# Optimization experiments

Hardware: AMD Instinct MI355X
Metric: run time of the kernel (lower is better)

## Reference

```python
import jax, jax.numpy as jnp
import numpy as np

DIM = 3072
HEADS = 24
HEAD_DIM = 128
SEQ = 4096
BATCH = 1
EPS = 1e-6


def setup_inputs() -> dict:
    key = jax.random.key(0)
    ks = jax.random.split(key, 12)
    s = 1.0 / np.sqrt(DIM)
    return {
        "hidden_states": jax.random.normal(ks[0], (BATCH, SEQ, DIM), dtype=jnp.float32),
        "cos": jax.random.uniform(ks[1], (SEQ, HEAD_DIM), dtype=jnp.float32, minval=-1.0, maxval=1.0),
        "sin": jax.random.uniform(ks[2], (SEQ, HEAD_DIM), dtype=jnp.float32, minval=-1.0, maxval=1.0),
        "Wq": jax.random.normal(ks[3], (DIM, HEADS * HEAD_DIM), dtype=jnp.float32) * s,
        "bq": jax.random.normal(ks[4], (HEADS * HEAD_DIM,), dtype=jnp.float32) * 0.02,
        "Wk": jax.random.normal(ks[5], (DIM, HEADS * HEAD_DIM), dtype=jnp.float32) * s,
        "bk": jax.random.normal(ks[6], (HEADS * HEAD_DIM,), dtype=jnp.float32) * 0.02,
        "Wv": jax.random.normal(ks[7], (DIM, HEADS * HEAD_DIM), dtype=jnp.float32) * s,
        "bv": jax.random.normal(ks[8], (HEADS * HEAD_DIM,), dtype=jnp.float32) * 0.02,
        "gq": jnp.ones((HEAD_DIM,), dtype=jnp.float32),
        "gk": jnp.ones((HEAD_DIM,), dtype=jnp.float32),
    }


def _rms_norm(x, g):
    # RMSNorm over last dim (head_dim), learnable scale g
    var = jnp.mean(jnp.square(x), axis=-1, keepdims=True)
    return x * jax.lax.rsqrt(var + EPS) * g


def _apply_rope(x, cos, sin):
    # x: [B, S, H, D]; cos/sin: [S, D]. Interleaved-pair rotation (Flux style).
    xr = x.reshape(*x.shape[:-1], HEAD_DIM // 2, 2)
    x_rot = jnp.stack((-xr[..., 1], xr[..., 0]), axis=-1).reshape(x.shape)
    c = cos[None, :, None, :]
    s = sin[None, :, None, :]
    return x * c + x_rot * s


def reference(hidden_states, cos, sin, Wq, bq, Wk, bk, Wv, bv, gq, gk):
    B, S, _ = hidden_states.shape
    q = (hidden_states @ Wq + bq).reshape(B, S, HEADS, HEAD_DIM)
    k = (hidden_states @ Wk + bk).reshape(B, S, HEADS, HEAD_DIM)
    v = (hidden_states @ Wv + bv).reshape(B, S, HEADS, HEAD_DIM)
    q = _apply_rope(_rms_norm(q, gq), cos, sin)
    k = _apply_rope(_rms_norm(k, gk), cos, sin)
    scale = 1.0 / jnp.sqrt(jnp.asarray(HEAD_DIM, dtype=q.dtype))
    scores = jnp.einsum("bqhd,bkhd->bhqk", q, k) * scale  # [B, H, S, S]
    probs = jax.nn.softmax(scores, axis=-1)
    out = jnp.einsum("bhqk,bkhd->bqhd", probs, v)  # [B, S, H, D]
    return out.reshape(B, S, HEADS * HEAD_DIM)
```

## Files before the change

kernel.cpp:

```cpp
#include <hip/hip_runtime.h>
#include <hip/hip_bf16.h>
#include <stdint.h>

#define DIM 3072
#define SEQ 4096
#define NH 24
#define HD 128

typedef __hip_bfloat16 bf16;
typedef __bf16 bfv8 __attribute__((ext_vector_type(8)));
typedef float f32x4 __attribute__((ext_vector_type(4)));
typedef float f32x16 __attribute__((ext_vector_type(16)));
typedef unsigned short us4 __attribute__((ext_vector_type(4)));
typedef unsigned short us8 __attribute__((ext_vector_type(8)));

template <int N> struct ic { static constexpr int value = N; };

__device__ __forceinline__ void async16(void* lds, const void* g) {
  __builtin_amdgcn_global_load_lds((const __attribute__((address_space(1))) void*)g,
                                   (__attribute__((address_space(3))) void*)lds, 16, 0, 0);
}

__device__ __forceinline__ unsigned short f2bf(float f) {
  unsigned int u = __builtin_bit_cast(unsigned int, f);
  u += 0x7fffu + ((u >> 16) & 1u);
  return (unsigned short)(u >> 16);
}
__device__ __forceinline__ float bf2f(unsigned short b) {
  return __builtin_bit_cast(float, (unsigned int)b << 16);
}
__device__ __forceinline__ unsigned int cvtpk(float lo, float hi) {
  unsigned int r;
  asm("v_cvt_pk_bf16_f32 %0, %1, %2" : "=v"(r) : "v"(lo), "v"(hi));
  return r;
}
__device__ __forceinline__ void pl32swap(unsigned int& a, unsigned int& b) {
  asm volatile("v_permlane32_swap_b32 %0, %1" : "+v"(a), "+v"(b));
}
#if __has_builtin(__builtin_amdgcn_exp2f)
__device__ __forceinline__ float fexp2(float x) { return __builtin_amdgcn_exp2f(x); }
#else
__device__ __forceinline__ float fexp2(float x) { return exp2f(x); }
#endif

#define MFMA16(a, b, c) __builtin_amdgcn_mfma_f32_16x16x32_bf16((a), (b), (c), 0, 0, 0)
#define MFMA32(a, b, c) __builtin_amdgcn_mfma_f32_32x32x16_bf16((a), (b), (c), 0, 0, 0)

__global__ __launch_bounds__(256) void k_cast(const float4* __restrict__ in,
                                              us4* __restrict__ o, int n4) {
  int i = blockIdx.x * 256 + threadIdx.x;
  if (i >= n4) return;
  float4 v = in[i];
  us4 r;
  r.x = f2bf(v.x); r.y = f2bf(v.y); r.z = f2bf(v.z); r.w = f2bf(v.w);
  o[i] = r;
}

__global__ __launch_bounds__(256) void k_transW(const float* __restrict__ W0,
    const float* __restrict__ W1, const float* __restrict__ W2,
    unsigned short* __restrict__ T0, unsigned short* __restrict__ T1,
    unsigned short* __restrict__ T2) {
  int z = blockIdx.z;
  const float* W = (z == 0) ? W0 : (z == 1) ? W1 : W2;
  unsigned short* T = (z == 0) ? T0 : (z == 1) ? T1 : T2;
  int kb = blockIdx.y * 64;
  int nb = blockIdx.x * 64;
  __shared__ float tile[64 * 64];
  int t = threadIdx.x;
#pragma unroll
  for (int p = 0; p < 4; ++p) {
    int cid = p * 256 + t;
    int row = cid >> 4, c4 = cid & 15;
    int slot = (c4 + (row >> 3)) & 15;
    float4 v = *(const float4*)&W[(size_t)(kb + row) * DIM + nb + c4 * 4];
    *(float4*)&tile[row * 64 + slot * 4] = v;
  }
  __syncthreads();
#pragma unroll
  for (int p = 0; p < 2; ++p) {
    int cid = p * 256 + t;
    int nl = cid >> 3, c8 = cid & 7;
    us8 o;
#pragma unroll
    for (int j = 0; j < 8; ++j) {
      int k = c8 * 8 + j;
      int slot = ((nl >> 2) + (k >> 3)) & 15;
      o[j] = f2bf(tile[k * 64 + slot * 4 + (nl & 3)]);
    }
    *(us8*)&T[(size_t)(nb + nl) * DIM + kb + c8 * 8] = o;
  }
}

__global__ __launch_bounds__(256, 3) void k_gemm(const unsigned short* __restrict__ A,
    const unsigned short* __restrict__ B0, const unsigned short* __restrict__ B1,
    const unsigned short* __restrict__ B2, const float* __restrict__ c0,
    const float* __restrict__ c1, const float* __restrict__ c2,
    const float* __restrict__ cosT, const float* __restrict__ sinT,
    const float* __restrict__ gq, const float* __restrict__ gk,
    unsigned short* __restrict__ o0, unsigned short* __restrict__ o1,
    unsigned short* __restrict__ o2) {
  const int b = blockIdx.x;
  const int yb = b % 32;
  const int r2b = b / 32;
  const int xb = r2b % 24;
  const int z = r2b / 24;
  const unsigned short* Bt = (z == 0) ? B0 : (z == 1) ? B1 : B2;
  const float* bias = (z == 0) ? c0 : (z == 1) ? c1 : c2;
  unsigned short* outp = (z == 0) ? o0 : (z == 1) ? o1 : o2;
  const int nb = xb * 128;
  const int mb = yb * 128;
  const int t = threadIdx.x;
  const int w = t >> 6, l = t & 63;
  const int wr = w >> 1, wc = w & 1;
  const int lq = l & 15, lg = l >> 4;
  __shared__ unsigned short lA[128 * 64];
  __shared__ unsigned short lB[128 * 64];
  __shared__ float lds_sq[128 * 2];
  f32x4 acc[4][4];
#pragma unroll
  for (int i = 0; i < 4; ++i)
#pragma unroll
    for (int j = 0; j < 4; ++j) acc[i][j] = (f32x4){0.f, 0.f, 0.f, 0.f};

  for (int kb = 0; kb < DIM; kb += 64) {
    __syncthreads();
#pragma unroll
    for (int r = 0; r < 4; ++r) {
      int row = (w * 4 + r) * 8 + (l >> 3);
      int sl = (l & 7) ^ (row & 7);
      async16(&lA[(w * 4 + r) * 512], A + (size_t)(mb + row) * DIM + kb + sl * 8);
      async16(&lB[(w * 4 + r) * 512], Bt + (size_t)(nb + row) * DIM + kb + sl * 8);
    }
    __syncthreads();
#pragma unroll
    for (int kc = 0; kc < 2; ++kc) {
      bfv8 af[4], bfv[4];
#pragma unroll
      for (int mf = 0; mf < 4; ++mf) {
        int row = wr * 64 + mf * 16 + lq;
        af[mf] = *(const bfv8*)&lA[row * 64 + (((kc * 4 + lg) ^ (row & 7)) * 8)];
      }
#pragma unroll
      for (int nf = 0; nf < 4; ++nf) {
        int row = wc * 64 + nf * 16 + lq;
        bfv[nf] = *(const bfv8*)&lB[row * 64 + (((kc * 4 + lg) ^ (row & 7)) * 8)];
      }
#pragma unroll
      for (int mf = 0; mf < 4; ++mf)
#pragma unroll
        for (int nf = 0; nf < 4; ++nf)
          acc[mf][nf] = MFMA16(af[mf], bfv[nf], acc[mf][nf]);
    }
  }

  float bv4[4];
#pragma unroll
  for (int nf = 0; nf < 4; ++nf) bv4[nf] = bias[nb + wc * 64 + nf * 16 + lq];
#pragma unroll
  for (int mf = 0; mf < 4; ++mf)
#pragma unroll
    for (int nf = 0; nf < 4; ++nf)
#pragma unroll
      for (int r = 0; r < 4; ++r) acc[mf][nf][r] += bv4[nf];

  const int hh = nb >> 7;
  unsigned short* obase0 = outp + (size_t)hh * SEQ * HD;

  if (z == 2) {
#pragma unroll
    for (int nf = 0; nf < 4; ++nf) {
      int dd = wc * 64 + nf * 16 + lq;
#pragma unroll
      for (int mf = 0; mf < 4; ++mf) {
        int srow = mb + wr * 64 + mf * 16 + lg * 4;
#pragma unroll
        for (int r = 0; r < 4; ++r)
          obase0[(size_t)(srow + r) * HD + dd] = f2bf(acc[mf][nf][r]);
      }
    }
    return;
  }

  float psum[4][4];
#pragma unroll
  for (int mf = 0; mf < 4; ++mf)
#pragma unroll
    for (int r = 0; r < 4; ++r) {
      float p = acc[mf][0][r] * acc[mf][0][r];
      p += acc[mf][1][r] * acc[mf][1][r];
      p += acc[mf][2][r] * acc[mf][2][r];
      p += acc[mf][3][r] * acc[mf][3][r];
      p += __shfl_xor(p, 1);
      p += __shfl_xor(p, 2);
      p += __shfl_xor(p, 4);
      p += __shfl_xor(p, 8);
      psum[mf][r] = p;
    }
  if (lq == 0) {
#pragma unroll
    for (int mf = 0; mf < 4; ++mf)
#pragma unroll
      for (int r = 0; r < 4; ++r)
        lds_sq[(wr * 64 + mf * 16 + lg * 4 + r) * 2 + wc] = psum[mf][r];
  }
  __syncthreads();

  const float* g = (z == 0) ? gq : gk;
  float gvec[4];
#pragma unroll
  for (int nf = 0; nf < 4; ++nf) gvec[nf] = g[wc * 64 + nf * 16 + lq];
  const float qs = (z == 0) ? 0.1275174373f : 1.0f;

#pragma unroll
  for (int mf = 0; mf < 4; ++mf)
#pragma unroll
    for (int r = 0; r < 4; ++r) {
      int row = wr * 64 + mf * 16 + lg * 4 + r;
      float tot = lds_sq[row * 2] + lds_sq[row * 2 + 1];
      float rrv = rsqrtf(tot * (1.0f / 128.0f) + 1e-6f);
      int s = mb + row;
#pragma unroll
      for (int nf = 0; nf < 4; ++nf) {
        int dd = wc * 64 + nf * 16 + lq;
        float y = acc[mf][nf][r] * rrv * gvec[nf];
        float yp = __shfl_xor(y, 1);
        float cc = cosT[s * HD + dd], sn = sinT[s * HD + dd];
        float o = (lq & 1) ? fmaf(yp, sn, y * cc) : fmaf(-yp, sn, y * cc);
        obase0[(size_t)s * HD + dd] = f2bf(o * qs);
      }
    }
}

__global__ __launch_bounds__(256) void k_transV(const unsigned short* __restrict__ vb,
                                                unsigned short* __restrict__ vt) {
  int hh = blockIdx.y;
  int sb = blockIdx.x * 64;
  __shared__ unsigned short tile[64 * 128];
  int t = threadIdx.x;
#pragma unroll
  for (int p = 0; p < 4; ++p) {
    int cid = p * 256 + t;
    int row = cid >> 4, c = cid & 15;
    int slot = (c + (row >> 3)) & 15;
    us8 v = *(const us8*)&vb[((size_t)hh * SEQ + sb + row) * HD + c * 8];
    *(us8*)&tile[row * 128 + slot * 8] = v;
  }
  __syncthreads();
#pragma unroll
  for (int p = 0; p < 4; ++p) {
    int cid = p * 256 + t;
    int d = cid >> 3, c8 = cid & 7;
    us8 o;
#pragma unroll
    for (int j = 0; j < 8; ++j) {
      int s = c8 * 8 + j;
      int slot = ((d >> 3) + (s >> 3)) & 15;
      o[j] = tile[s * 128 + slot * 8 + (d & 7)];
    }
    *(us8*)&vt[((size_t)hh * HD + d) * SEQ + sb + c8 * 8] = o;
  }
}

__global__ __launch_bounds__(256, 2) void k_attn(const unsigned short* __restrict__ qg,
    const unsigned short* __restrict__ kg, const unsigned short* __restrict__ vtg,
    float* __restrict__ outp) {
  const int bflat = blockIdx.x;
  const int h = bflat % 24;
  const int qb0 = (bflat / 24) * 128;
  const int t = threadIdx.x;
  const int w = t >> 6, l = t & 63;
  const int l31 = l & 31, hi = l >> 5;

  __shared__ unsigned short lKf[2 * 8192];
  __shared__ unsigned short lVf[2 * 8192];

  bfv8 qf[8];
  {
    const unsigned short* qrow = qg + ((size_t)h * SEQ + qb0 + w * 32 + l31) * HD + hi * 8;
#pragma unroll
    for (int ks = 0; ks < 8; ++ks) qf[ks] = *(const bfv8*)(qrow + ks * 16);
  }

  int kidx[8], vidx[4][2];
#pragma unroll
  for (int ks = 0; ks < 8; ++ks)
    kidx[ks] = l31 * 128 + (((ks * 2 + hi) ^ (l31 & 7) ^ ((l31 >> 3) & 1)) * 8);
#pragma unroll
  for (int dt = 0; dt < 4; ++dt)
#pragma unroll
    for (int ksub = 0; ksub < 2; ++ksub)
      vidx[dt][ksub] =
          (dt * 32 + l31) * 32 + (((ksub * 2 + hi) ^ (l31 & 3) ^ ((l31 >> 2) & 3)) * 8);

  const unsigned short *kp0, *kp1, *vp0, *vp1;
  {
    int kr0 = w * 4 + (l >> 4), kr1 = 16 + kr0;
    kp0 = kg + ((size_t)h * SEQ + kr0) * HD + (((l & 15) ^ (kr0 & 7) ^ ((kr0 >> 3) & 1)) * 8);
    kp1 = kg + ((size_t)h * SEQ + kr1) * HD + (((l & 15) ^ (kr1 & 7) ^ ((kr1 >> 3) & 1)) * 8);
    int vr0 = w * 16 + (l >> 2), vr1 = 64 + vr0;
    vp0 = vtg + ((size_t)h * HD + vr0) * SEQ + (((l & 3) ^ (vr0 & 3) ^ ((vr0 >> 2) & 3)) * 8);
    vp1 = vtg + ((size_t)h * HD + vr1) * SEQ + (((l & 3) ^ (vr1 & 3) ^ ((vr1 >> 2) & 3)) * 8);
  }

#define STAGE(B)                                                              \
  do {                                                                        \
    async16(&lKf[(B) * 8192 + w * 512], kp0);                                 \
    async16(&lKf[(B) * 8192 + 2048 + w * 512], kp1);                          \
    async16(&lKf[(B) * 8192 + 4096 + w * 512], kp0 + 32 * HD);                \
    async16(&lKf[(B) * 8192 + 6144 + w * 512], kp1 + 32 * HD);                \
    async16(&lVf[(B) * 8192 + w * 512], vp0);                                 \
    async16(&lVf[(B) * 8192 + 2048 + w * 512], vp1);                          \
    async16(&lVf[(B) * 8192 + 4096 + w * 512], vp0 + 32);                     \
    async16(&lVf[(B) * 8192 + 6144 + w * 512], vp1 + 32);                     \
    kp0 += 64 * HD; kp1 += 64 * HD; vp0 += 64; vp1 += 64;                     \
  } while (0)

  f32x16 oacc[4];
#pragma unroll
  for (int dt = 0; dt < 4; ++dt)
#pragma unroll
    for (int r = 0; r < 16; ++r) oacc[dt][r] = 0.f;
  float l_run = 0.f;

  STAGE(0);

  auto phase = [&](auto bufc, auto stagec) {
    constexpr int CUR = decltype(bufc)::value;
    constexpr int DOSTAGE = decltype(stagec)::value;
    asm volatile("s_waitcnt vmcnt(0)" ::: "memory");
    __builtin_amdgcn_s_barrier();
    __builtin_amdgcn_sched_barrier(0);
    if constexpr (DOSTAGE) STAGE(CUR ^ 1);
    __builtin_amdgcn_sched_barrier(0);

    f32x16 sa, sb;
#pragma unroll
    for (int r = 0; r < 16; ++r) { sa[r] = 0.f; sb[r] = 0.f; }
    __builtin_amdgcn_s_setprio(1);
#pragma unroll
    for (int ks = 0; ks < 8; ++ks) {
      bfv8 kfa = *(const bfv8*)&lKf[CUR * 8192 + kidx[ks]];
      bfv8 kfb = *(const bfv8*)&lKf[CUR * 8192 + 4096 + kidx[ks]];
      sa = MFMA32(kfa, qf[ks], sa);
      sb = MFMA32(kfb, qf[ks], sb);
    }
    __builtin_amdgcn_s_setprio(0);

#pragma unroll
    for (int r = 0; r < 16; ++r) { sa[r] = fexp2(sa[r]); sb[r] = fexp2(sb[r]); }
    {
      float a0 = (sa[0] + sa[1]) + (sa[2] + sa[3]);
      float a1 = (sa[4] + sa[5]) + (sa[6] + sa[7]);
      float a2 = (sa[8] + sa[9]) + (sa[10] + sa[11]);
      float a3 = (sa[12] + sa[13]) + (sa[14] + sa[15]);
      float b0 = (sb[0] + sb[1]) + (sb[2] + sb[3]);
      float b1 = (sb[4] + sb[5]) + (sb[6] + sb[7]);
      float b2 = (sb[8] + sb[9]) + (sb[10] + sb[11]);
      float b3 = (sb[12] + sb[13]) + (sb[14] + sb[15]);
      l_run += ((a0 + a1) + (a2 + a3)) + ((b0 + b1) + (b2 + b3));
    }

    bfv8 paA[2], paB[2];
    {
      unsigned int a0 = cvtpk(sa[0], sa[1]), a1 = cvtpk(sa[2], sa[3]);
      unsigned int b0 = cvtpk(sa[4], sa[5]), b1 = cvtpk(sa[6], sa[7]);
      unsigned int c0 = cvtpk(sa[8], sa[9]), c1 = cvtpk(sa[10], sa[11]);
      unsigned int d0 = cvtpk(sa[12], sa[13]), d1 = cvtpk(sa[14], sa[15]);
      pl32swap(a0, b0); pl32swap(a1, b1); pl32swap(c0, d0); pl32swap(c1, d1);
      paA[0] = __builtin_bit_cast(bfv8, make_uint4(a0, a1, b0, b1));
      paA[1] = __builtin_bit_cast(bfv8, make_uint4(c0, c1, d0, d1));
      a0 = cvtpk(sb[0], sb[1]); a1 = cvtpk(sb[2], sb[3]);
      b0 = cvtpk(sb[4], sb[5]); b1 = cvtpk(sb[6], sb[7]);
      c0 = cvtpk(sb[8], sb[9]); c1 = cvtpk(sb[10], sb[11]);
      d0 = cvtpk(sb[12], sb[13]); d1 = cvtpk(sb[14], sb[15]);
      pl32swap(a0, b0); pl32swap(a1, b1); pl32swap(c0, d0); pl32swap(c1, d1);
      paB[0] = __builtin_bit_cast(bfv8, make_uint4(a0, a1, b0, b1));
      paB[1] = __builtin_bit_cast(bfv8, make_uint4(c0, c1, d0, d1));
    }

    __builtin_amdgcn_s_setprio(1);
#pragma unroll
    for (int dt = 0; dt < 4; ++dt) {
#pragma unroll
      for (int ksub = 0; ksub < 2; ++ksub) {
        bfv8 vfa = *(const bfv8*)&lVf[CUR * 8192 + vidx[dt][ksub]];
        oacc[dt] = MFMA32(paA[ksub], vfa, oacc[dt]);
      }
#pragma unroll
      for (int ksub = 0; ksub < 2; ++ksub) {
        bfv8 vfb = *(const bfv8*)&lVf[CUR * 8192 + 4096 + vidx[dt][ksub]];
        oacc[dt] = MFMA32(paB[ksub], vfb, oacc[dt]);
      }
    }
    __builtin_amdgcn_s_setprio(0);
  };

  for (int it = 0; it < 31; ++it) {
    phase(ic<0>{}, ic<1>{});
    phase(ic<1>{}, ic<1>{});
  }
  phase(ic<0>{}, ic<1>{});
  phase(ic<1>{}, ic<0>{});

  l_run += __shfl_xor(l_run, 32);
  float linv = 1.0f / l_run;
#pragma unroll
  for (int r = 0; r < 16; ++r) {
    int qr = (r & 3) + 8 * (r >> 2) + 4 * hi;
    float lr = __shfl(linv, qr);
    float* orow = outp + (size_t)(qb0 + w * 32 + qr) * DIM + h * HD;
#pragma unroll
    for (int dt = 0; dt < 4; ++dt) orow[dt * 32 + l31] = oacc[dt][r] * lr;
  }
#undef STAGE
}

extern "C" void kernel_launch(void* const* d_in, const int* in_sizes, int n_in,
                              void* d_out, int out_size, void* d_ws, size_t ws_size,
                              hipStream_t stream) {
  const float* hs = (const float*)d_in[0];
  const float* cosT = (const float*)d_in[1];
  const float* sinT = (const float*)d_in[2];
  const float* Wq = (const float*)d_in[3];
  const float* bq = (const float*)d_in[4];
  const float* Wk = (const float*)d_in[5];
  const float* bk = (const float*)d_in[6];
  const float* Wv = (const float*)d_in[7];
  const float* bv = (const float*)d_in[8];
  const float* gq = (const float*)d_in[9];
  const float* gk = (const float*)d_in[10];
  float* out = (float*)d_out;

  char* ws = (char*)d_ws;
  const size_t SZ_HS = (size_t)SEQ * DIM * 2;
  const size_t SZ_W = (size_t)DIM * DIM * 2;
  const size_t SZ_HEAD = (size_t)NH * SEQ * HD * 2;
  unsigned short* hsb = (unsigned short*)ws;               ws += SZ_HS;
  unsigned short* WqT = (unsigned short*)ws;               ws += SZ_W;
  unsigned short* WkT = (unsigned short*)ws;               ws += SZ_W;
  unsigned short* WvT = (unsigned short*)ws;               ws += SZ_W;
  unsigned short* q_b = (unsigned short*)ws;               ws += SZ_HEAD;
  unsigned short* k_b = (unsigned short*)ws;               ws += SZ_HEAD;
  unsigned short* v_b = (unsigned short*)ws;               ws += SZ_HEAD;
  unsigned short* vtr = (unsigned short*)ws;               ws += SZ_HEAD;

  int n4 = SEQ * DIM / 4;
  k_cast<<<dim3(n4 / 256), dim3(256), 0, stream>>>((const float4*)hs, (us4*)hsb, n4);
  k_transW<<<dim3(48, 48, 3), dim3(256), 0, stream>>>(Wq, Wk, Wv, WqT, WkT, WvT);
  k_gemm<<<dim3(2304), dim3(256), 0, stream>>>(hsb, WqT, WkT, WvT, bq, bk, bv,
                                               cosT, sinT, gq, gk, q_b, k_b, v_b);
  k_transV<<<dim3(64, 24), dim3(256), 0, stream>>>(v_b, vtr);
  k_attn<<<dim3(768), dim3(256), 0, stream>>>(q_b, k_b, vtr, out);
}
```

Baseline: 517.2 us.

## Fuse input cast into weight-transpose kernel and write V transposed from GEMM

Merges the hidden-state bf16 cast into the weight transpose launch as an extra z-slice, and has the QKV GEMM epilogue write V directly in [head, d, seq] layout so the separate V transpose kernel is removed. This drops two launches and one full read/write pass over V. The direct transposed store writes 8-byte chunks strided by SEQ, so it is less coalesced than the old row-major store.

```diff
diff --git a/kernel.cpp b/kernel.cpp
--- a/kernel.cpp
+++ b/kernel.cpp
@@ -46,27 +46,29 @@
 #define MFMA16(a, b, c) __builtin_amdgcn_mfma_f32_16x16x32_bf16((a), (b), (c), 0, 0, 0)
 #define MFMA32(a, b, c) __builtin_amdgcn_mfma_f32_32x32x16_bf16((a), (b), (c), 0, 0, 0)
 
-__global__ __launch_bounds__(256) void k_cast(const float4* __restrict__ in,
-                                              us4* __restrict__ o, int n4) {
-  int i = blockIdx.x * 256 + threadIdx.x;
-  if (i >= n4) return;
-  float4 v = in[i];
-  us4 r;
-  r.x = f2bf(v.x); r.y = f2bf(v.y); r.z = f2bf(v.z); r.w = f2bf(v.w);
-  o[i] = r;
-}
-
-__global__ __launch_bounds__(256) void k_transW(const float* __restrict__ W0,
-    const float* __restrict__ W1, const float* __restrict__ W2,
-    unsigned short* __restrict__ T0, unsigned short* __restrict__ T1,
-    unsigned short* __restrict__ T2) {
+__global__ __launch_bounds__(256) void k_prep(const float* __restrict__ hs,
+    us4* __restrict__ hsb, const float* __restrict__ W0, const float* __restrict__ W1,
+    const float* __restrict__ W2, unsigned short* __restrict__ T0,
+    unsigned short* __restrict__ T1, unsigned short* __restrict__ T2) {
   int z = blockIdx.z;
+  int t = threadIdx.x;
+  if (z == 3) {
+    const int n4 = SEQ * DIM / 4;
+    const int stride = 48 * 48 * 256;
+    const float4* in = (const float4*)hs;
+    for (int i = (blockIdx.y * 48 + blockIdx.x) * 256 + t; i < n4; i += stride) {
+      float4 v = in[i];
+      us4 r;
+      r.x = f2bf(v.x); r.y = f2bf(v.y); r.z = f2bf(v.z); r.w = f2bf(v.w);
+      hsb[i] = r;
+    }
+    return;
+  }
   const float* W = (z == 0) ? W0 : (z == 1) ? W1 : W2;
   unsigned short* T = (z == 0) ? T0 : (z == 1) ? T1 : T2;
   int kb = blockIdx.y * 64;
   int nb = blockIdx.x * 64;
   __shared__ float tile[64 * 64];
-  int t = threadIdx.x;
 #pragma unroll
   for (int p = 0; p < 4; ++p) {
     int cid = p * 256 + t;
@@ -164,22 +166,25 @@
       for (int r = 0; r < 4; ++r) acc[mf][nf][r] += bv4[nf];
 
   const int hh = nb >> 7;
-  unsigned short* obase0 = outp + (size_t)hh * SEQ * HD;
 
   if (z == 2) {
+    unsigned short* vbase = outp + (size_t)hh * HD * SEQ;
 #pragma unroll
     for (int nf = 0; nf < 4; ++nf) {
       int dd = wc * 64 + nf * 16 + lq;
 #pragma unroll
       for (int mf = 0; mf < 4; ++mf) {
-        int srow = mb + wr * 64 + mf * 16 + lg * 4;
-#pragma unroll
-        for (int r = 0; r < 4; ++r)
-          obase0[(size_t)(srow + r) * HD + dd] = f2bf(acc[mf][nf][r]);
+        int s0 = mb + wr * 64 + mf * 16 + lg * 4;
+        us4 pk;
+#pragma unroll
+        for (int r = 0; r < 4; ++r) pk[r] = f2bf(acc[mf][nf][r]);
+        *(us4*)&vbase[(size_t)dd * SEQ + s0] = pk;
       }
     }
     return;
   }
+
+  unsigned short* obase0 = outp + (size_t)hh * SEQ * HD;
 
   float psum[4][4];
 #pragma unroll
@@ -229,36 +234,6 @@
         obase0[(size_t)s * HD + dd] = f2bf(o * qs);
       }
     }
-}
-
-__global__ __launch_bounds__(256) void k_transV(const unsigned short* __restrict__ vb,
-                                                unsigned short* __restrict__ vt) {
-  int hh = blockIdx.y;
-  int sb = blockIdx.x * 64;
-  __shared__ unsigned short tile[64 * 128];
-  int t = threadIdx.x;
-#pragma unroll
-  for (int p = 0; p < 4; ++p) {
-    int cid = p * 256 + t;
-    int row = cid >> 4, c = cid & 15;
-    int slot = (c + (row >> 3)) & 15;
-    us8 v = *(const us8*)&vb[((size_t)hh * SEQ + sb + row) * HD + c * 8];
-    *(us8*)&tile[row * 128 + slot * 8] = v;
-  }
-  __syncthreads();
-#pragma unroll
-  for (int p = 0; p < 4; ++p) {
-    int cid = p * 256 + t;
-    int d = cid >> 3, c8 = cid & 7;
-    us8 o;
-#pragma unroll
-    for (int j = 0; j < 8; ++j) {
-      int s = c8 * 8 + j;
-      int slot = ((d >> 3) + (s >> 3)) & 15;
-      o[j] = tile[s * 128 + slot * 8 + (d & 7)];
-    }
-    *(us8*)&vt[((size_t)hh * HD + d) * SEQ + sb + c8 * 8] = o;
-  }
 }
 
 __global__ __launch_bounds__(256, 2) void k_attn(const unsigned short* __restrict__ qg,
@@ -441,14 +416,11 @@
   unsigned short* WvT = (unsigned short*)ws;               ws += SZ_W;
   unsigned short* q_b = (unsigned short*)ws;               ws += SZ_HEAD;
   unsigned short* k_b = (unsigned short*)ws;               ws += SZ_HEAD;
-  unsigned short* v_b = (unsigned short*)ws;               ws += SZ_HEAD;
   unsigned short* vtr = (unsigned short*)ws;               ws += SZ_HEAD;
 
-  int n4 = SEQ * DIM / 4;
-  k_cast<<<dim3(n4 / 256), dim3(256), 0, stream>>>((const float4*)hs, (us4*)hsb, n4);
-  k_transW<<<dim3(48, 48, 3), dim3(256), 0, stream>>>(Wq, Wk, Wv, WqT, WkT, WvT);
+  k_prep<<<dim3(48, 48, 4), dim3(256), 0, stream>>>(hs, (us4*)hsb, Wq, Wk, Wv,
+                                                    WqT, WkT, WvT);
   k_gemm<<<dim3(2304), dim3(256), 0, stream>>>(hsb, WqT, WkT, WvT, bq, bk, bv,
-                                               cosT, sinT, gq, gk, q_b, k_b, v_b);
-  k_transV<<<dim3(64, 24), dim3(256), 0, stream>>>(v_b, vtr);
+                                               cosT, sinT, gq, gk, q_b, k_b, vtr);
   k_attn<<<dim3(768), dim3(256), 0, stream>>>(q_b, k_b, vtr, out);
 }
```

Result: no change. 508.5 us (median of 2 runs) (-1.7%).
